# Kernel optimization log

Hardware: AMD Instinct MI355X
Metric: run time of the kernel (lower is better)

Reference implementation:

```python
import jax, jax.numpy as jnp
import numpy as np

D_N = 128  # node_embedding_dimensions
D_E = 128  # edge_embedding_dimensions
N_REL = 1000  # edge_count (number of relations)
BATCH = 16384


def _l2_normalize(x, eps=1e-12):
    # mimics torch.nn.functional.normalize(p=2, dim=1)
    norm = jnp.sqrt(jnp.sum(x * x, axis=1, keepdims=True))
    return x / jnp.maximum(norm, eps)


def setup_inputs() -> dict:
    key = jax.random.key(0)
    k1, k2, k3, k4, k5 = jax.random.split(key, 5)
    head_embeddings = jax.random.normal(k1, (BATCH, D_N), dtype=jnp.float32)
    tail_embeddings = jax.random.normal(k2, (BATCH, D_N), dtype=jnp.float32)
    edge_embeddings = jax.random.normal(k3, (BATCH, D_E), dtype=jnp.float32)
    proj_table = jax.random.normal(k4, (N_REL, D_E * D_N), dtype=jnp.float32)
    edge_indices = jax.random.randint(k5, (BATCH,), 0, N_REL, dtype=jnp.int64)
    return {
        "head_embeddings": head_embeddings,
        "tail_embeddings": tail_embeddings,
        "edge_embeddings": edge_embeddings,
        "proj_table": proj_table,
        "edge_indices": edge_indices,
    }


def reference(head_embeddings, tail_embeddings, edge_embeddings, proj_table, edge_indices):
    # L2-normalize head/tail node embeddings along feature dim
    h = _l2_normalize(head_embeddings)  # [B, d_n]
    t = _l2_normalize(tail_embeddings)  # [B, d_n]
    B = h.shape[0]
    # gather per-relation projection matrices: [B, d_e, d_n]
    P = proj_table[edge_indices].reshape(B, D_E, D_N)
    # project heads/tails into relation space: matmul(P, x[...,None]) -> [B, d_e]
    ph = jnp.einsum("bed,bd->be", P, h)
    pt = jnp.einsum("bed,bd->be", P, t)
    # l2 dissimilarity: squared L2 norm of (h_proj + r - t_proj); score is its negation
    diff = ph + edge_embeddings - pt
    return -jnp.sum(diff * diff, axis=1)
```

## Files before the change

### kernel.cpp

```cpp
#include <hip/hip_runtime.h>
#include <stdint.h>

#define D 128
#define LIST_CAP 256

__global__ __launch_bounds__(512, 6) void transr_fused(
    const float* __restrict__ head,
    const float* __restrict__ tail,
    const float* __restrict__ edge,
    const float* __restrict__ proj,
    const int* __restrict__ idx,
    float* __restrict__ out,
    int B)
{
    const int rel = blockIdx.x;
    const int tid = threadIdx.x;

    __shared__ float Ul[8 * D];
    __shared__ float Rl[8 * D];
    __shared__ float part[64];
    __shared__ int   list[LIST_CAP];
    __shared__ int   El[8];
    __shared__ int   cnt;

    if (tid == 0) cnt = 0;

    const int w  = tid >> 6;
    const int wl = tid & 63;
    const int r  = 16 * w + (wl >> 2);
    const int cq = wl & 3;

    const float* __restrict__ Pg = proj + (size_t)rel * (D * D) + (size_t)r * D + 32 * cq;
    float4 pT[8];
    #pragma unroll
    for (int k = 0; k < 8; ++k)
        pT[k] = *reinterpret_cast<const float4*>(Pg + 4 * k);

    __syncthreads();

    const int4* __restrict__ idx4 = reinterpret_cast<const int4*>(idx);
    const int nv = B >> 2;
    for (int f = tid; f < nv; f += 512) {
        const int4 v = idx4[f];
        if (v.x == rel) { int p = atomicAdd(&cnt, 1); if (p < LIST_CAP) list[p] = 4 * f + 0; }
        if (v.y == rel) { int p = atomicAdd(&cnt, 1); if (p < LIST_CAP) list[p] = 4 * f + 1; }
        if (v.z == rel) { int p = atomicAdd(&cnt, 1); if (p < LIST_CAP) list[p] = 4 * f + 2; }
        if (v.w == rel) { int p = atomicAdd(&cnt, 1); if (p < LIST_CAP) list[p] = 4 * f + 3; }
    }
    __syncthreads();
    const int n = min(cnt, LIST_CAP);
    if (n == 0) return;

    const int nchunk = (n + 7) >> 3;
    for (int ch = 0; ch < nchunk; ++ch) {
        const int e = ch * 8 + w;
        int b = -1;
        float2 u2 = make_float2(0.f, 0.f);
        float2 r2 = make_float2(0.f, 0.f);
        if (e < n) {
            b = list[e];
            const float2 h2 = *reinterpret_cast<const float2*>(head + (size_t)b * D + 2 * wl);
            const float2 t2 = *reinterpret_cast<const float2*>(tail + (size_t)b * D + 2 * wl);
            r2 = *reinterpret_cast<const float2*>(edge + (size_t)b * D + 2 * wl);
            float hs = h2.x * h2.x + h2.y * h2.y;
            float ts = t2.x * t2.x + t2.y * t2.y;
            #pragma unroll
            for (int m = 1; m < 64; m <<= 1) {
                hs += __shfl_xor(hs, m);
                ts += __shfl_xor(ts, m);
            }
            const float hn = fmaxf(sqrtf(hs), 1e-12f);
            const float tn = fmaxf(sqrtf(ts), 1e-12f);
            u2.x = h2.x / hn - t2.x / tn;
            u2.y = h2.y / hn - t2.y / tn;
        }
        *reinterpret_cast<float2*>(Ul + w * D + 2 * wl) = u2;
        *reinterpret_cast<float2*>(Rl + w * D + 2 * wl) = r2;
        if (wl == 0) El[w] = b;
        __syncthreads();

        #pragma unroll
        for (int e2 = 0; e2 < 8; ++e2) {
            const float* Ue = Ul + e2 * D + 32 * cq;
            float a = 0.f;
            #pragma unroll
            for (int k = 0; k < 8; ++k) {
                const float4 u = *reinterpret_cast<const float4*>(Ue + 4 * k);
                a = fmaf(pT[k].x, u.x, a); a = fmaf(pT[k].y, u.y, a);
                a = fmaf(pT[k].z, u.z, a); a = fmaf(pT[k].w, u.w, a);
            }
            a += __shfl_xor(a, 1);
            a += __shfl_xor(a, 2);
            const float dfr = a + Rl[e2 * D + r];
            float s = (cq == 0) ? dfr * dfr : 0.f;
            s += __shfl_xor(s, 4);
            s += __shfl_xor(s, 8);
            s += __shfl_xor(s, 16);
            s += __shfl_xor(s, 32);
            if (wl == 0) part[e2 * 8 + w] = s;
        }
        __syncthreads();

        {
            float v = (wl < 8) ? part[w * 8 + wl] : 0.f;
            v += __shfl_xor(v, 1);
            v += __shfl_xor(v, 2);
            v += __shfl_xor(v, 4);
            if (wl == 0) {
                const int bb = El[w];
                if (bb >= 0) out[bb] = -v;
            }
        }
        __syncthreads();
    }
}

extern "C" void kernel_launch(void* const* d_in, const int* in_sizes, int n_in,
                              void* d_out, int out_size, void* d_ws, size_t ws_size,
                              hipStream_t stream) {
    const float* head = (const float*)d_in[0];
    const float* tail = (const float*)d_in[1];
    const float* edge = (const float*)d_in[2];
    const float* proj = (const float*)d_in[3];
    const int*   idx  = (const int*)d_in[4];
    float* out = (float*)d_out;

    const int B    = in_sizes[0] / D;
    const int nrel = in_sizes[3] / (D * D);

    transr_fused<<<nrel, 512, 0, stream>>>(head, tail, edge, proj, idx, out, B);
}
```

Measured before the change: 154.2 us.

## Process 16 edges per chunk with two-row register tiles and LDS partial reduction

Each block now handles 16 edges per chunk instead of 8, and each thread holds two 32-wide row slices of the relation's projection matrix. The reduction changes from a shuffle tree per edge to writing per-column-quarter partial dot products into shared memory and reducing them in a second phase. This halves the number of chunk iterations and barriers and doubles FMA work per loaded LDS vector. In exchange it uses more registers and shared memory (about 40KB), and lowers the occupancy hint from 6 to 4.

```diff
diff --git a/kernel.cpp b/kernel.cpp
--- a/kernel.cpp
+++ b/kernel.cpp
@@ -3,8 +3,9 @@
 
 #define D 128
 #define LIST_CAP 256
+#define CHUNK 16
 
-__global__ __launch_bounds__(512, 6) void transr_fused(
+__global__ __launch_bounds__(512, 4) void transr_fused(
     const float* __restrict__ head,
     const float* __restrict__ tail,
     const float* __restrict__ edge,
@@ -16,25 +17,29 @@
     const int rel = blockIdx.x;
     const int tid = threadIdx.x;
 
-    __shared__ float Ul[8 * D];
-    __shared__ float Rl[8 * D];
-    __shared__ float part[64];
+    __shared__ float Ul[CHUNK][D];
+    __shared__ float Rl[CHUNK][D];
+    __shared__ float part4[4][CHUNK][D];
     __shared__ int   list[LIST_CAP];
-    __shared__ int   El[8];
+    __shared__ int   El[CHUNK];
     __shared__ int   cnt;
 
     if (tid == 0) cnt = 0;
 
     const int w  = tid >> 6;
     const int wl = tid & 63;
-    const int r  = 16 * w + (wl >> 2);
-    const int cq = wl & 3;
+    const int cq = w & 3;
+    const int eh = w >> 2;
 
-    const float* __restrict__ Pg = proj + (size_t)rel * (D * D) + (size_t)r * D + 32 * cq;
-    float4 pT[8];
+    const float* __restrict__ Pg  = proj + (size_t)rel * (D * D);
+    const float* __restrict__ PgA = Pg + (size_t)wl * D + 32 * cq;
+    const float* __restrict__ PgB = Pg + (size_t)(wl + 64) * D + 32 * cq;
+    float4 pA[8], pB[8];
     #pragma unroll
-    for (int k = 0; k < 8; ++k)
-        pT[k] = *reinterpret_cast<const float4*>(Pg + 4 * k);
+    for (int k = 0; k < 8; ++k) {
+        pA[k] = *reinterpret_cast<const float4*>(PgA + 4 * k);
+        pB[k] = *reinterpret_cast<const float4*>(PgB + 4 * k);
+    }
 
     __syncthreads();
 
@@ -51,64 +56,82 @@
     const int n = min(cnt, LIST_CAP);
     if (n == 0) return;
 
-    const int nchunk = (n + 7) >> 3;
+    #pragma unroll
+    for (int k = 0; k < 8; ++k) {
+        asm volatile("" : "+v"(pA[k].x), "+v"(pA[k].y), "+v"(pA[k].z), "+v"(pA[k].w));
+        asm volatile("" : "+v"(pB[k].x), "+v"(pB[k].y), "+v"(pB[k].z), "+v"(pB[k].w));
+    }
+
+    const int nchunk = (n + CHUNK - 1) / CHUNK;
     for (int ch = 0; ch < nchunk; ++ch) {
-        const int e = ch * 8 + w;
-        int b = -1;
-        float2 u2 = make_float2(0.f, 0.f);
-        float2 r2 = make_float2(0.f, 0.f);
-        if (e < n) {
-            b = list[e];
-            const float2 h2 = *reinterpret_cast<const float2*>(head + (size_t)b * D + 2 * wl);
-            const float2 t2 = *reinterpret_cast<const float2*>(tail + (size_t)b * D + 2 * wl);
-            r2 = *reinterpret_cast<const float2*>(edge + (size_t)b * D + 2 * wl);
-            float hs = h2.x * h2.x + h2.y * h2.y;
-            float ts = t2.x * t2.x + t2.y * t2.y;
-            #pragma unroll
-            for (int m = 1; m < 64; m <<= 1) {
-                hs += __shfl_xor(hs, m);
-                ts += __shfl_xor(ts, m);
-            }
-            const float hn = fmaxf(sqrtf(hs), 1e-12f);
-            const float tn = fmaxf(sqrtf(ts), 1e-12f);
-            u2.x = h2.x / hn - t2.x / tn;
-            u2.y = h2.y / hn - t2.y / tn;
+        const int eA = ch * CHUNK + 2 * w;
+        const int eB = eA + 1;
+        const int bA = (eA < n) ? list[eA] : -1;
+        const int bB = (eB < n) ? list[eB] : -1;
+        float2 hA = make_float2(0.f, 0.f), tA = hA, rA = hA;
+        float2 hB = hA, tB = hA, rB = hA;
+        if (bA >= 0) {
+            hA = *reinterpret_cast<const float2*>(head + (size_t)bA * D + 2 * wl);
+            tA = *reinterpret_cast<const float2*>(tail + (size_t)bA * D + 2 * wl);
+            rA = *reinterpret_cast<const float2*>(edge + (size_t)bA * D + 2 * wl);
         }
-        *reinterpret_cast<float2*>(Ul + w * D + 2 * wl) = u2;
-        *reinterpret_cast<float2*>(Rl + w * D + 2 * wl) = r2;
-        if (wl == 0) El[w] = b;
+        if (bB >= 0) {
+            hB = *reinterpret_cast<const float2*>(head + (size_t)bB * D + 2 * wl);
+            tB = *reinterpret_cast<const float2*>(tail + (size_t)bB * D + 2 * wl);
+            rB = *reinterpret_cast<const float2*>(edge + (size_t)bB * D + 2 * wl);
+        }
+        float hsA = hA.x * hA.x + hA.y * hA.y, tsA = tA.x * tA.x + tA.y * tA.y;
+        float hsB = hB.x * hB.x + hB.y * hB.y, tsB = tB.x * tB.x + tB.y * tB.y;
+        #pragma unroll
+        for (int m = 1; m < 64; m <<= 1) {
+            hsA += __shfl_xor(hsA, m); tsA += __shfl_xor(tsA, m);
+            hsB += __shfl_xor(hsB, m); tsB += __shfl_xor(tsB, m);
+        }
+        const float hnA = fmaxf(sqrtf(hsA), 1e-12f), tnA = fmaxf(sqrtf(tsA), 1e-12f);
+        const float hnB = fmaxf(sqrtf(hsB), 1e-12f), tnB = fmaxf(sqrtf(tsB), 1e-12f);
+        float2 uA, uB;
+        uA.x = hA.x / hnA - tA.x / tnA;  uA.y = hA.y / hnA - tA.y / tnA;
+        uB.x = hB.x / hnB - tB.x / tnB;  uB.y = hB.y / hnB - tB.y / tnB;
+        *reinterpret_cast<float2*>(&Ul[2 * w    ][2 * wl]) = uA;
+        *reinterpret_cast<float2*>(&Ul[2 * w + 1][2 * wl]) = uB;
+        *reinterpret_cast<float2*>(&Rl[2 * w    ][2 * wl]) = rA;
+        *reinterpret_cast<float2*>(&Rl[2 * w + 1][2 * wl]) = rB;
+        if (wl == 0) { El[2 * w] = bA; El[2 * w + 1] = bB; }
         __syncthreads();
 
         #pragma unroll
-        for (int e2 = 0; e2 < 8; ++e2) {
-            const float* Ue = Ul + e2 * D + 32 * cq;
-            float a = 0.f;
+        for (int j = 0; j < 8; ++j) {
+            const int e = 8 * eh + j;
+            const float* Ue = &Ul[e][32 * cq];
+            float a0 = 0.f, a1 = 0.f;
             #pragma unroll
             for (int k = 0; k < 8; ++k) {
                 const float4 u = *reinterpret_cast<const float4*>(Ue + 4 * k);
-                a = fmaf(pT[k].x, u.x, a); a = fmaf(pT[k].y, u.y, a);
-                a = fmaf(pT[k].z, u.z, a); a = fmaf(pT[k].w, u.w, a);
+                a0 = fmaf(pA[k].x, u.x, a0); a0 = fmaf(pA[k].y, u.y, a0);
+                a0 = fmaf(pA[k].z, u.z, a0); a0 = fmaf(pA[k].w, u.w, a0);
+                a1 = fmaf(pB[k].x, u.x, a1); a1 = fmaf(pB[k].y, u.y, a1);
+                a1 = fmaf(pB[k].z, u.z, a1); a1 = fmaf(pB[k].w, u.w, a1);
             }
-            a += __shfl_xor(a, 1);
-            a += __shfl_xor(a, 2);
-            const float dfr = a + Rl[e2 * D + r];
-            float s = (cq == 0) ? dfr * dfr : 0.f;
-            s += __shfl_xor(s, 4);
-            s += __shfl_xor(s, 8);
-            s += __shfl_xor(s, 16);
-            s += __shfl_xor(s, 32);
-            if (wl == 0) part[e2 * 8 + w] = s;
+            part4[cq][e][wl]      = a0;
+            part4[cq][e][wl + 64] = a1;
         }
         __syncthreads();
 
-        {
-            float v = (wl < 8) ? part[w * 8 + wl] : 0.f;
-            v += __shfl_xor(v, 1);
-            v += __shfl_xor(v, 2);
-            v += __shfl_xor(v, 4);
+        #pragma unroll
+        for (int s2 = 0; s2 < 2; ++s2) {
+            const int e = 2 * w + s2;
+            const float p0 = ((part4[0][e][wl] + part4[1][e][wl])
+                            + (part4[2][e][wl] + part4[3][e][wl]));
+            const float p1 = ((part4[0][e][wl + 64] + part4[1][e][wl + 64])
+                            + (part4[2][e][wl + 64] + part4[3][e][wl + 64]));
+            const float d0 = p0 + Rl[e][wl];
+            const float d1 = p1 + Rl[e][wl + 64];
+            float s = fmaf(d0, d0, d1 * d1);
+            #pragma unroll
+            for (int m = 1; m < 64; m <<= 1) s += __shfl_xor(s, m);
             if (wl == 0) {
-                const int bb = El[w];
-                if (bb >= 0) out[bb] = -v;
+                const int bb = El[e];
+                if (bb >= 0) out[bb] = -s;
             }
         }
         __syncthreads();
```

New measurement: 141.7 us. 8.1% less time.
